# Kernel tuning notes

Measured on AMD Instinct MI355X. Metric: run time of the kernel, lower is better.

Reference implementation:

```python
import jax, jax.numpy as jnp
import numpy as np

C_S, C_Z, MAX_LEN, N_AA, L = 256, 128, 1024, 21, 512
LN_EPS = 1e-5


def setup_inputs() -> dict:
    key = jax.random.key(0)
    ks = jax.random.split(key, 12)
    inp = {
        "seq": jax.random.randint(ks[0], (L,), 0, N_AA),
        "chain_id_res": jax.random.randint(ks[1], (L,), 0, 2),
        "res_idx": jax.random.randint(ks[2], (L,), 0, L),
        # learned parameters
        "E_aa": jax.random.normal(ks[3], (N_AA, C_S), jnp.float32) * 0.02,
        "E_pos": jax.random.normal(ks[4], (MAX_LEN, C_S), jnp.float32) * 0.02,
        "E_chain": jax.random.normal(ks[5], (2, C_S), jnp.float32) * 0.02,
        "E_chainpair": jax.random.normal(ks[6], (4, C_Z), jnp.float32) * 0.02,
        "E_relpos": jax.random.normal(ks[7], (66, C_Z), jnp.float32) * 0.02,
        "W_pair": jax.random.normal(ks[8], (3 * C_S, C_Z), jnp.float32) / np.sqrt(3 * C_S),
        "b_pair": jnp.zeros((C_Z,), jnp.float32),
        "ln_w": jnp.ones((C_S,), jnp.float32),
        "ln_b": jnp.zeros((C_S,), jnp.float32),
    }
    return inp


def reference(seq, chain_id_res, res_idx, E_aa, E_pos, E_chain, E_chainpair,
              E_relpos, W_pair, b_pair, ln_w, ln_b):
    # single rep: sum of three embedding lookups -> [L, c_s]
    s = E_aa[seq] + E_pos[res_idx] + E_chain[chain_id_res]

    # LayerNorm over last dim
    mu = jnp.mean(s, axis=-1, keepdims=True)
    var = jnp.mean(jnp.square(s - mu), axis=-1, keepdims=True)
    u = (s - mu) * jax.lax.rsqrt(var + LN_EPS) * ln_w + ln_b  # [L, c_s]

    # pair_proj(cat(u_i, u_j, u_i*u_j)) decomposed: W = [W1; W2; W3]
    W1, W2, W3 = W_pair[:C_S], W_pair[C_S:2 * C_S], W_pair[2 * C_S:]
    zi = u @ W1                                   # [L, c_z] per-i term
    zj = u @ W2                                   # [L, c_z] per-j term
    zx = jnp.einsum('ic,jc,cz->ijz', u, u, W3)    # cross term (u_i*u_j) @ W3
    z = zi[:, None, :] + zj[None, :, :] + zx + b_pair  # [L, L, c_z]

    # chain-pair and relative-position embeddings
    chain_pair = chain_id_res[:, None] * 2 + chain_id_res[None, :]  # [L, L] in [0,3]
    same_chain = chain_id_res[:, None] == chain_id_res[None, :]
    diff = res_idx[:, None] - res_idx[None, :]
    clipped = jnp.clip(diff, -32, 32) + 32
    relpos = jnp.where(same_chain, clipped, 65)  # cross-chain bucket = 65

    z = z + E_chainpair[chain_pair] + E_relpos[relpos]
    return s, z
```

## Files before the change

### kernel.cpp

```cpp
#include <hip/hip_runtime.h>
#include <hip/hip_bf16.h>

#define L 512
#define CS 256
#define CZ 128
#define LN_EPS 1e-5f

typedef _Float16 f16_t;
typedef f16_t f16x8 __attribute__((ext_vector_type(8)));
typedef float f32x4 __attribute__((ext_vector_type(4)));

__global__ __launch_bounds__(256) void k_prep(
    const int* __restrict__ seq, const int* __restrict__ cid,
    const int* __restrict__ ridx,
    const float* __restrict__ Eaa, const float* __restrict__ Epos,
    const float* __restrict__ Ech, const float* __restrict__ lnw,
    const float* __restrict__ lnb, const float* __restrict__ Wp,
    const float* __restrict__ bp, const float* __restrict__ Ecp,
    const float* __restrict__ Erp,
    float* __restrict__ s_out, f16_t* __restrict__ u2,
    float* __restrict__ zrow, float* __restrict__ zcol,
    f16_t* __restrict__ w3c, float* __restrict__ tab)
{
    __shared__ float su[CS];
    __shared__ float red[8];
    const int i = blockIdx.x;
    const int c = threadIdx.x;

    if (i < 128) {
        w3c[(c >> 3) * (CZ * 8) + i * 8 + (c & 7)] = (f16_t)Wp[(2 * CS + c) * CZ + i];
    } else if (i < 128 + 264) {
        const int b2 = i - 128;
        if (c < CZ)
            tab[b2 * CZ + c] = Ecp[(b2 / 66) * CZ + c] + Erp[(b2 % 66) * CZ + c];
    }

    const int sq = seq[i], ri = ridx[i], ci = cid[i];
    const float v = Eaa[sq * CS + c] + Epos[ri * CS + c] + Ech[ci * CS + c];
    s_out[i * CS + c] = v;

    float s1 = v, s2 = v * v;
    #pragma unroll
    for (int o = 32; o > 0; o >>= 1) {
        s1 += __shfl_down(s1, o, 64);
        s2 += __shfl_down(s2, o, 64);
    }
    const int wv = c >> 6, lane = c & 63;
    if (lane == 0) { red[wv * 2] = s1; red[wv * 2 + 1] = s2; }
    __syncthreads();
    const float S  = red[0] + red[2] + red[4] + red[6];
    const float SS = red[1] + red[3] + red[5] + red[7];
    const float mu  = S * (1.0f / CS);
    const float var = SS * (1.0f / CS) - mu * mu;
    const float rs  = rsqrtf(var + LN_EPS);
    const float u   = (v - mu) * rs * lnw[c] + lnb[c];
    u2[(c >> 3) * (L * 8) + i * 8 + (c & 7)] = (f16_t)u;
    su[c] = u;
    __syncthreads();

    const int z = c & 127;
    const int half = c >> 7;
    const float* W = Wp + half * CS * CZ + z;
    float a0 = 0, a1 = 0, a2 = 0, a3 = 0;
    #pragma unroll 8
    for (int cc = 0; cc < CS; cc += 4) {
        a0 += su[cc + 0] * W[(cc + 0) * CZ];
        a1 += su[cc + 1] * W[(cc + 1) * CZ];
        a2 += su[cc + 2] * W[(cc + 2) * CZ];
        a3 += su[cc + 3] * W[(cc + 3) * CZ];
    }
    const float acc = (a0 + a1) + (a2 + a3);
    if (half) zcol[i * CZ + z] = acc;
    else      zrow[i * CZ + z] = acc + bp[z];
}

__global__ __launch_bounds__(512, 4) void k_pair(
    const f16_t* __restrict__ u2, const f16_t* __restrict__ w3c,
    const float* __restrict__ zrow, const float* __restrict__ zcol,
    const float* __restrict__ tab,
    const int* __restrict__ cid, const int* __restrict__ ridx,
    float* __restrict__ zout)
{
    __shared__ f16_t lds[(1024 + 256) * 8];
    f16x8* lj = (f16x8*)lds;
    f16x8* li = ((f16x8*)lds) + 1024;

    const int t = threadIdx.x;
    const int lane = t & 63, wave = t >> 6;
    const int m = lane & 15, q = lane >> 4;
    const int j0 = blockIdx.x * 32, i0 = blockIdx.y * 8;
    const int jh = wave & 1;
    const int ih = (wave >> 1) & 1;
    const int zh = wave >> 2;
    const int jm = j0 + jh * 16 + m;
    const int ib = ih * 4;
    const int zb = zh * 64;

    const f16x8* pu = (const f16x8*)u2;
    const f16x8* pw = (const f16x8*)w3c;

    if (t < 256) li[t] = pu[(t >> 3) * L + i0 + (t & 7)];
    #pragma unroll
    for (int rep = 0; rep < 2; ++rep) {
        const int un = rep * 512 + t;
        lj[un] = pu[(un >> 5) * L + j0 + (un & 31)];
    }

    const int cj = cid[jm], rj = ridx[jm];
    int xx[4];
    #pragma unroll
    for (int ii = 0; ii < 4; ++ii) {
        const int i = i0 + ib + ii;
        const int ci = cid[i], ri = ridx[i];
        int d = ri - rj; d = d < -32 ? -32 : (d > 32 ? 32 : d);
        xx[ii] = ((ci * 2 + cj) * 66) + ((ci == cj) ? (d + 32) : 65);
    }

    __syncthreads();

    #pragma unroll 1
    for (int pass = 0; pass < 2; ++pass) {
        const int z0 = zb + pass * 32;

        f32x4 acc[4][2];
        #pragma unroll
        for (int ii = 0; ii < 4; ++ii) {
            acc[ii][0] = (f32x4){0.f, 0.f, 0.f, 0.f};
            acc[ii][1] = (f32x4){0.f, 0.f, 0.f, 0.f};
        }

        #pragma unroll 2
        for (int k32 = 0; k32 < 8; ++k32) {
            const int cb = k32 * 4 + q;
            const f16x8 A0 = pw[cb * CZ + z0 + m];
            const f16x8 A1 = pw[cb * CZ + z0 + 16 + m];
            const f16x8 ujv = lj[cb * 32 + jh * 16 + m];
            #pragma unroll
            for (int ii = 0; ii < 4; ++ii) {
                const f16x8 B = li[cb * 8 + ib + ii] * ujv;
                acc[ii][0] = __builtin_amdgcn_mfma_f32_16x16x32_f16(A0, B, acc[ii][0], 0, 0, 0);
                acc[ii][1] = __builtin_amdgcn_mfma_f32_16x16x32_f16(A1, B, acc[ii][1], 0, 0, 0);
            }
        }

        const int zo0 = z0 + q * 4;
        const int zo1 = z0 + 16 + q * 4;
        const f32x4 ZC0 = *(const f32x4*)&zcol[jm * CZ + zo0];
        const f32x4 ZC1 = *(const f32x4*)&zcol[jm * CZ + zo1];
        #pragma unroll
        for (int ii = 0; ii < 4; ++ii) {
            const int i = i0 + ib + ii;
            float* r_o = zout + ((size_t)i * L + jm) * CZ;
            const f32x4 zr0 = *(const f32x4*)&zrow[i * CZ + zo0];
            const f32x4 zr1 = *(const f32x4*)&zrow[i * CZ + zo1];
            const f32x4 tb0 = *(const f32x4*)&tab[xx[ii] * CZ + zo0];
            const f32x4 tb1 = *(const f32x4*)&tab[xx[ii] * CZ + zo1];
            *(f32x4*)(r_o + zo0) = acc[ii][0] + zr0 + ZC0 + tb0;
            *(f32x4*)(r_o + zo1) = acc[ii][1] + zr1 + ZC1 + tb1;
        }
    }
}

extern "C" void kernel_launch(void* const* d_in, const int* in_sizes, int n_in,
                              void* d_out, int out_size, void* d_ws, size_t ws_size,
                              hipStream_t stream) {
    const int*   seq  = (const int*)d_in[0];
    const int*   cid  = (const int*)d_in[1];
    const int*   ridx = (const int*)d_in[2];
    const float* Eaa  = (const float*)d_in[3];
    const float* Epos = (const float*)d_in[4];
    const float* Ech  = (const float*)d_in[5];
    const float* Ecp  = (const float*)d_in[6];
    const float* Erp  = (const float*)d_in[7];
    const float* Wp   = (const float*)d_in[8];
    const float* bp   = (const float*)d_in[9];
    const float* lnw  = (const float*)d_in[10];
    const float* lnb  = (const float*)d_in[11];

    float* out   = (float*)d_out;
    float* s_out = out;
    float* zout  = out + L * CS;

    char* ws = (char*)d_ws;
    f16_t* u2   = (f16_t*)ws;
    f16_t* w3c  = (f16_t*)(ws + 262144);
    float* zrow = (float*)(ws + 327680);
    float* zcol = (float*)(ws + 589824);
    float* tab  = (float*)(ws + 851968);

    hipLaunchKernelGGL(k_prep, dim3(L), dim3(256), 0, stream,
                       seq, cid, ridx, Eaa, Epos, Ech, lnw, lnb, Wp, bp,
                       Ecp, Erp, s_out, u2, zrow, zcol, w3c, tab);
    hipLaunchKernelGGL(k_pair, dim3(16, 64), dim3(512), 0, stream,
                       u2, w3c, zrow, zcol, tab, cid, ridx, zout);
}
```

Baseline: 183.3 us.

## Remap pair waves to z-slices, keep W3 fragments in registers, preload epilogue into accumulators

Each of the eight waves now owns a 16-wide z slice across all 32 j and 8 i of the tile, instead of splitting j, i and z across waves. This lets it hold its W3 A-fragments in registers for the whole block, rather than reloading them from global memory in every k step. The additive terms (zrow, zcol, chain/relpos table) are loaded into the accumulators before the MFMA loop, so the epilogue becomes plain stores. The cost is more live registers (eight A fragments plus the preloaded accumulators), and each store now covers a 16-float z segment per row rather than 32-float runs.

Result: slower. 236.5 us (+29.0%).

```diff
diff --git a/kernel.cpp b/kernel.cpp
--- a/kernel.cpp
+++ b/kernel.cpp
@@ -89,12 +89,8 @@
     const int lane = t & 63, wave = t >> 6;
     const int m = lane & 15, q = lane >> 4;
     const int j0 = blockIdx.x * 32, i0 = blockIdx.y * 8;
-    const int jh = wave & 1;
-    const int ih = (wave >> 1) & 1;
-    const int zh = wave >> 2;
-    const int jm = j0 + jh * 16 + m;
-    const int ib = ih * 4;
-    const int zb = zh * 64;
+    const int zseg = wave * 16;
+    const int zq = zseg + q * 4;
 
     const f16x8* pu = (const f16x8*)u2;
     const f16x8* pw = (const f16x8*)w3c;
@@ -106,57 +102,59 @@
         lj[un] = pu[(un >> 5) * L + j0 + (un & 31)];
     }
 
-    const int cj = cid[jm], rj = ridx[jm];
-    int xx[4];
+    f16x8 A[8];
     #pragma unroll
-    for (int ii = 0; ii < 4; ++ii) {
-        const int i = i0 + ib + ii;
-        const int ci = cid[i], ri = ridx[i];
-        int d = ri - rj; d = d < -32 ? -32 : (d > 32 ? 32 : d);
-        xx[ii] = ((ci * 2 + cj) * 66) + ((ci == cj) ? (d + 32) : 65);
-    }
+    for (int k32 = 0; k32 < 8; ++k32)
+        A[k32] = pw[(k32 * 4 + q) * CZ + zseg + m];
+
+    const int ja = j0 + m, jb = j0 + 16 + m;
+    const int cja = cid[ja], rja = ridx[ja];
+    const int cjb = cid[jb], rjb = ridx[jb];
+    const f32x4 ZCa = *(const f32x4*)&zcol[ja * CZ + zq];
+    const f32x4 ZCb = *(const f32x4*)&zcol[jb * CZ + zq];
 
     __syncthreads();
 
     #pragma unroll 1
-    for (int pass = 0; pass < 2; ++pass) {
-        const int z0 = zb + pass * 32;
+    for (int g = 0; g < 2; ++g) {
+        const int ibase = i0 + g * 4;
 
         f32x4 acc[4][2];
         #pragma unroll
         for (int ii = 0; ii < 4; ++ii) {
-            acc[ii][0] = (f32x4){0.f, 0.f, 0.f, 0.f};
-            acc[ii][1] = (f32x4){0.f, 0.f, 0.f, 0.f};
+            const int i = ibase + ii;
+            const int ci = cid[i], ri = ridx[i];
+            int d;
+            d = ri - rja; d = d < -32 ? -32 : (d > 32 ? 32 : d);
+            const int xa = ((ci * 2 + cja) * 66) + ((ci == cja) ? (d + 32) : 65);
+            d = ri - rjb; d = d < -32 ? -32 : (d > 32 ? 32 : d);
+            const int xb = ((ci * 2 + cjb) * 66) + ((ci == cjb) ? (d + 32) : 65);
+            const f32x4 zr = *(const f32x4*)&zrow[i * CZ + zq];
+            acc[ii][0] = zr + ZCa + *(const f32x4*)&tab[xa * CZ + zq];
+            acc[ii][1] = zr + ZCb + *(const f32x4*)&tab[xb * CZ + zq];
         }
 
-        #pragma unroll 2
+        #pragma unroll
         for (int k32 = 0; k32 < 8; ++k32) {
             const int cb = k32 * 4 + q;
-            const f16x8 A0 = pw[cb * CZ + z0 + m];
-            const f16x8 A1 = pw[cb * CZ + z0 + 16 + m];
-            const f16x8 ujv = lj[cb * 32 + jh * 16 + m];
+            const f16x8 uja = lj[cb * 32 + m];
+            const f16x8 ujb = lj[cb * 32 + 16 + m];
             #pragma unroll
             for (int ii = 0; ii < 4; ++ii) {
-                const f16x8 B = li[cb * 8 + ib + ii] * ujv;
-                acc[ii][0] = __builtin_amdgcn_mfma_f32_16x16x32_f16(A0, B, acc[ii][0], 0, 0, 0);
-                acc[ii][1] = __builtin_amdgcn_mfma_f32_16x16x32_f16(A1, B, acc[ii][1], 0, 0, 0);
+                const f16x8 ui = li[cb * 8 + g * 4 + ii];
+                acc[ii][0] = __builtin_amdgcn_mfma_f32_16x16x32_f16(
+                    A[k32], ui * uja, acc[ii][0], 0, 0, 0);
+                acc[ii][1] = __builtin_amdgcn_mfma_f32_16x16x32_f16(
+                    A[k32], ui * ujb, acc[ii][1], 0, 0, 0);
             }
         }
 
-        const int zo0 = z0 + q * 4;
-        const int zo1 = z0 + 16 + q * 4;
-        const f32x4 ZC0 = *(const f32x4*)&zcol[jm * CZ + zo0];
-        const f32x4 ZC1 = *(const f32x4*)&zcol[jm * CZ + zo1];
         #pragma unroll
         for (int ii = 0; ii < 4; ++ii) {
-            const int i = i0 + ib + ii;
-            float* r_o = zout + ((size_t)i * L + jm) * CZ;
-            const f32x4 zr0 = *(const f32x4*)&zrow[i * CZ + zo0];
-            const f32x4 zr1 = *(const f32x4*)&zrow[i * CZ + zo1];
-            const f32x4 tb0 = *(const f32x4*)&tab[xx[ii] * CZ + zo0];
-            const f32x4 tb1 = *(const f32x4*)&tab[xx[ii] * CZ + zo1];
-            *(f32x4*)(r_o + zo0) = acc[ii][0] + zr0 + ZC0 + tb0;
-            *(f32x4*)(r_o + zo1) = acc[ii][1] + zr1 + ZC1 + tb1;
+            const int i = ibase + ii;
+            float* r = zout + ((size_t)i * L + ja) * CZ + zq;
+            *(f32x4*)r = acc[ii][0];
+            *(f32x4*)(r + 16 * CZ) = acc[ii][1];
         }
     }
 }
```
